# Optimization experiments

Hardware: AMD Instinct MI355X
Metric: run time of the kernel (lower is better)

Reference implementation:

```python
import jax, jax.numpy as jnp
import numpy as np

EPS = 1e-8  # matches torch F.cosine_similarity eps


def setup_inputs() -> dict:
    key = jax.random.key(0)
    S, U, D = 2048, 10, 256  # speakers, utterances/speaker, embedding dim
    embeddings = jax.random.normal(key, (S * U, D), dtype=jnp.float32)
    labels = jnp.repeat(jnp.arange(S, dtype=jnp.int64), U)  # speaker-blocked, as the view() assumes
    return {"embeddings": embeddings, "labels": labels}


def reference(embeddings, labels):
    labels_np = np.asarray(labels)
    S = int(np.unique(labels_np).size)          # num_speakers (static)
    B, D = embeddings.shape
    U = B // S                                   # num_utterances
    E = embeddings.reshape(S, U, D)
    C = E.mean(axis=1)                           # (S, D) centroids
    En = E / jnp.maximum(jnp.linalg.norm(E, axis=-1, keepdims=True), EPS)
    Cn = C / jnp.maximum(jnp.linalg.norm(C, axis=-1, keepdims=True), EPS)
    sim = jnp.einsum('sud,kd->suk', En, Cn)      # (S, U, S) cosine similarities
    idx = jnp.arange(S)
    pos = sim[idx, :, idx]                       # (S, U) similarity to own centroid
    neg_mask = jnp.eye(S, dtype=bool)[:, None, :]  # mask out k == i
    neg = jnp.where(neg_mask, -jnp.inf, sim)
    lse = jax.nn.logsumexp(neg, axis=-1)         # (S, U)
    loss = jnp.mean(-pos + lse)
    return loss
```

## Files before the change

### kernel.cpp

```cpp
#include <hip/hip_runtime.h>
#include <math.h>

#define SS   2048
#define UU   10
#define DD   256
#define BB   (SS * UU)
#define EPSF 1e-8f

typedef __attribute__((ext_vector_type(8))) short   bf16x8;
typedef __attribute__((ext_vector_type(4))) float   floatx4;

__device__ static inline unsigned short f2bf(float f) {
    union { float f; unsigned u; } v; v.f = f;
    unsigned r = (v.u + 0x7FFFu + ((v.u >> 16) & 1u)) >> 16;
    return (unsigned short)r;
}

__device__ static inline void gl_lds16(const unsigned short* g, unsigned short* l) {
    __builtin_amdgcn_global_load_lds((const __attribute__((address_space(1))) void*)g,
                                     (__attribute__((address_space(3))) void*)l, 16, 0, 0);
}

__global__ __launch_bounds__(256) void prep_kernel(const float* __restrict__ E,
                                                   unsigned short* __restrict__ Enb,
                                                   unsigned short* __restrict__ Cnb,
                                                   float* __restrict__ sumexp,
                                                   float* __restrict__ out) {
    const int s   = blockIdx.x;
    const int wid = threadIdx.x >> 6, lane = threadIdx.x & 63;
    __shared__ float cent[4][256];
    __shared__ float sred[256];

    if (threadIdx.x < UU) sumexp[s * UU + threadIdx.x] = 0.f;
    if (s == 0 && threadIdx.x == 0) out[0] = 0.f;

    float cp0 = 0.f, cp1 = 0.f, cp2 = 0.f, cp3 = 0.f;
    for (int u = wid; u < UU; u += 4) {
        const size_t roff = (size_t)(s * UU + u) * DD;
        float4 v = ((const float4*)(E + roff))[lane];
        float ssq = v.x * v.x + v.y * v.y + v.z * v.z + v.w * v.w;
#pragma unroll
        for (int off = 32; off; off >>= 1) ssq += __shfl_xor(ssq, off, 64);
        const float rinv = 1.0f / fmaxf(sqrtf(ssq), EPSF);
        ushort4 o;
        o.x = f2bf(v.x * rinv); o.y = f2bf(v.y * rinv);
        o.z = f2bf(v.z * rinv); o.w = f2bf(v.w * rinv);
        ((ushort4*)(Enb + roff))[lane] = o;
        cp0 += v.x; cp1 += v.y; cp2 += v.z; cp3 += v.w;
    }
    cent[wid][lane * 4 + 0] = cp0;
    cent[wid][lane * 4 + 1] = cp1;
    cent[wid][lane * 4 + 2] = cp2;
    cent[wid][lane * 4 + 3] = cp3;
    __syncthreads();

    const int d = threadIdx.x;
    const float c = (cent[0][d] + cent[1][d] + cent[2][d] + cent[3][d]) * 0.1f;
    sred[d] = c * c;
    __syncthreads();
#pragma unroll
    for (int off = 128; off; off >>= 1) {
        if (d < off) sred[d] += sred[d + off];
        __syncthreads();
    }
    const float rinv = 1.0f / fmaxf(sqrtf(sred[0]), EPSF);
    Cnb[(size_t)s * DD + d] = f2bf(c * rinv);
}

#define BM 128
#define BN 128
#define BK 32

__global__ __launch_bounds__(256) void gemm_lse_kernel(const unsigned short* __restrict__ Enb,
                                                       const unsigned short* __restrict__ Cnb,
                                                       float* __restrict__ posArr,
                                                       float* __restrict__ sumexp) {
    __shared__ unsigned short As[BM * BK];
    __shared__ unsigned short Bs[BN * BK];

    const int tid  = threadIdx.x;
    const int wid  = tid >> 6, lane = tid & 63;
    const int l15  = lane & 15, quad = lane >> 4;
    const int wave_m = wid >> 1, wave_n = wid & 1;

    const int bn = blockIdx.x & 15;
    const int bm = blockIdx.x >> 4;
    const int row0 = bm * BM, n0 = bn * BN;

    const int rl = lane >> 2;
    const int gf = ((lane & 3) ^ ((rl >> 1) & 3)) * 8;
    const unsigned short* gp[4];
    unsigned short* lp[4];
#pragma unroll
    for (int i = 0; i < 4; ++i) {
        const int c = wid * 4 + i;
        if (c < 8) {
            gp[i] = Enb + (size_t)(row0 + c * 16 + rl) * DD + gf;
            lp[i] = As + c * 512;
        } else {
            gp[i] = Cnb + (size_t)(n0 + (c - 8) * 16 + rl) * DD + gf;
            lp[i] = Bs + (c - 8) * 512;
        }
    }

    const int fswz = (quad ^ ((l15 >> 1) & 3)) * 8;
    int aoff[4], boff[4];
#pragma unroll
    for (int t = 0; t < 4; ++t) {
        aoff[t] = (wave_m * 64 + t * 16 + l15) * BK + fswz;
        boff[t] = (wave_n * 64 + t * 16 + l15) * BK + fswz;
    }

    floatx4 acc[4][4];
#pragma unroll
    for (int i = 0; i < 4; ++i)
#pragma unroll
        for (int j = 0; j < 4; ++j) acc[i][j] = (floatx4){0.f, 0.f, 0.f, 0.f};

    for (int k0 = 0; k0 < DD; k0 += BK) {
        __syncthreads();
#pragma unroll
        for (int i = 0; i < 4; ++i) gl_lds16(gp[i] + k0, lp[i]);
        __syncthreads();

        bf16x8 af[4], bfr[4];
#pragma unroll
        for (int t = 0; t < 4; ++t) af[t]  = *(const bf16x8*)(As + aoff[t]);
#pragma unroll
        for (int t = 0; t < 4; ++t) bfr[t] = *(const bf16x8*)(Bs + boff[t]);
#pragma unroll
        for (int mt = 0; mt < 4; ++mt)
#pragma unroll
            for (int nt = 0; nt < 4; ++nt)
                acc[mt][nt] = __builtin_amdgcn_mfma_f32_16x16x32_bf16(af[mt], bfr[nt], acc[mt][nt], 0, 0, 0);
    }

#pragma unroll
    for (int mt = 0; mt < 4; ++mt) {
        float rs[4] = {0.f, 0.f, 0.f, 0.f};
        const int growb = row0 + wave_m * 64 + mt * 16 + quad * 4;
#pragma unroll
        for (int nt = 0; nt < 4; ++nt) {
            const int col = n0 + wave_n * 64 + nt * 16 + l15;
#pragma unroll
            for (int r = 0; r < 4; ++r) {
                const int grow = growb + r;
                const float sim = acc[mt][nt][r];
                if (col == grow / UU) {
                    posArr[grow] = sim;
                } else {
                    rs[r] += __expf(sim);
                }
            }
        }
#pragma unroll
        for (int m = 1; m < 16; m <<= 1) {
#pragma unroll
            for (int r = 0; r < 4; ++r) rs[r] += __shfl_xor(rs[r], m, 64);
        }
        if (l15 == 0) {
#pragma unroll
            for (int r = 0; r < 4; ++r) atomicAdd(&sumexp[growb + r], rs[r]);
        }
    }
}

__global__ __launch_bounds__(256) void finalize_kernel(const float* __restrict__ posArr,
                                                       const float* __restrict__ sumexp,
                                                       float* __restrict__ out) {
    __shared__ float sred[256];
    const int tid = threadIdx.x;
    const int r = blockIdx.x * 256 + tid;
    sred[tid] = logf(sumexp[r]) - posArr[r];
    __syncthreads();
#pragma unroll
    for (int off = 128; off; off >>= 1) {
        if (tid < off) sred[tid] += sred[tid + off];
        __syncthreads();
    }
    if (tid == 0) atomicAdd(out, sred[0] * (1.0f / (float)BB));
}

extern "C" void kernel_launch(void* const* d_in, const int* in_sizes, int n_in,
                              void* d_out, int out_size, void* d_ws, size_t ws_size,
                              hipStream_t stream) {
    const float* E = (const float*)d_in[0];
    float* out = (float*)d_out;

    unsigned short* Enb = (unsigned short*)d_ws;
    unsigned short* Cnb = Enb + (size_t)BB * DD;
    float* posArr = (float*)(Cnb + (size_t)SS * DD);
    float* sumexp = posArr + BB;

    prep_kernel<<<SS, 256, 0, stream>>>(E, Enb, Cnb, sumexp, out);
    gemm_lse_kernel<<<(BB / BM) * (SS / BN), 256, 0, stream>>>(Enb, Cnb, posArr, sumexp);
    finalize_kernel<<<BB / 256, 256, 0, stream>>>(posArr, sumexp, out);
}
```

Before: 115.6 us.

## Preload full K into LDS and pipeline MFMA with per-chunk vmcnt waits

Each block now issues all eight K-chunk global→LDS loads up front into a 128 KB LDS buffer, then consumes chunks in order, waiting on vmcnt counters so MFMA work on early chunks overlaps the remaining loads. This removes the per-iteration load/sync serialization of the single-buffered loop. It also remaps block indices with a swizzle so that concurrently running blocks share A/B tiles, aiming for better L2 reuse. The large LDS footprint limits occupancy to about one block per CU.

```diff
diff --git a/kernel.cpp b/kernel.cpp
--- a/kernel.cpp
+++ b/kernel.cpp
@@ -70,21 +70,39 @@
 #define BM 128
 #define BN 128
 #define BK 32
+#define NCK 8
+
+__device__ __forceinline__ void chunk_mfma(const unsigned short* Ab,
+                                           const unsigned short* Bb,
+                                           const int* aoff, const int* boff,
+                                           floatx4 (&acc)[4][4]) {
+    bf16x8 af[4], bfr[4];
+#pragma unroll
+    for (int t = 0; t < 4; ++t) af[t]  = *(const bf16x8*)(Ab + aoff[t]);
+#pragma unroll
+    for (int t = 0; t < 4; ++t) bfr[t] = *(const bf16x8*)(Bb + boff[t]);
+#pragma unroll
+    for (int mt = 0; mt < 4; ++mt)
+#pragma unroll
+        for (int nt = 0; nt < 4; ++nt)
+            acc[mt][nt] = __builtin_amdgcn_mfma_f32_16x16x32_bf16(af[mt], bfr[nt], acc[mt][nt], 0, 0, 0);
+}
 
 __global__ __launch_bounds__(256) void gemm_lse_kernel(const unsigned short* __restrict__ Enb,
                                                        const unsigned short* __restrict__ Cnb,
                                                        float* __restrict__ posArr,
                                                        float* __restrict__ sumexp) {
-    __shared__ unsigned short As[BM * BK];
-    __shared__ unsigned short Bs[BN * BK];
+    __shared__ unsigned short As[NCK * BM * BK];
+    __shared__ unsigned short Bs[NCK * BN * BK];
 
     const int tid  = threadIdx.x;
     const int wid  = tid >> 6, lane = tid & 63;
     const int l15  = lane & 15, quad = lane >> 4;
     const int wave_m = wid >> 1, wave_n = wid & 1;
 
-    const int bn = blockIdx.x & 15;
-    const int bm = blockIdx.x >> 4;
+    const int swz = (blockIdx.x & 7) * 320 + (blockIdx.x >> 3);
+    const int bn = swz & 15;
+    const int bm = swz >> 4;
     const int row0 = bm * BM, n0 = bn * BN;
 
     const int rl = lane >> 2;
@@ -103,6 +121,13 @@
         }
     }
 
+#pragma unroll
+    for (int ck = 0; ck < NCK; ++ck) {
+#pragma unroll
+        for (int i = 0; i < 4; ++i)
+            gl_lds16(gp[i] + ck * BK, lp[i] + ck * (BM * BK));
+    }
+
     const int fswz = (quad ^ ((l15 >> 1) & 3)) * 8;
     int aoff[4], boff[4];
 #pragma unroll
@@ -117,23 +142,15 @@
 #pragma unroll
         for (int j = 0; j < 4; ++j) acc[i][j] = (floatx4){0.f, 0.f, 0.f, 0.f};
 
-    for (int k0 = 0; k0 < DD; k0 += BK) {
-        __syncthreads();
-#pragma unroll
-        for (int i = 0; i < 4; ++i) gl_lds16(gp[i] + k0, lp[i]);
-        __syncthreads();
-
-        bf16x8 af[4], bfr[4];
-#pragma unroll
-        for (int t = 0; t < 4; ++t) af[t]  = *(const bf16x8*)(As + aoff[t]);
-#pragma unroll
-        for (int t = 0; t < 4; ++t) bfr[t] = *(const bf16x8*)(Bs + boff[t]);
-#pragma unroll
-        for (int mt = 0; mt < 4; ++mt)
-#pragma unroll
-            for (int nt = 0; nt < 4; ++nt)
-                acc[mt][nt] = __builtin_amdgcn_mfma_f32_16x16x32_bf16(af[mt], bfr[nt], acc[mt][nt], 0, 0, 0);
-    }
+#define STEP(CK, VM)                                                        \
+    asm volatile("s_waitcnt vmcnt(" #VM ")" ::: "memory");                  \
+    __builtin_amdgcn_s_barrier();                                           \
+    __builtin_amdgcn_sched_barrier(0);                                      \
+    chunk_mfma(As + (CK) * (BM * BK), Bs + (CK) * (BN * BK), aoff, boff, acc);
+
+    STEP(0, 28) STEP(1, 24) STEP(2, 20) STEP(3, 16)
+    STEP(4, 12) STEP(5, 8)  STEP(6, 4)  STEP(7, 0)
+#undef STEP
 
 #pragma unroll
     for (int mt = 0; mt < 4; ++mt) {
```

Result: slower. 153.7 us (+33.0%).

## Rewrite GEMM-LSE with 256x256 tiles, double-buffered LDS pipeline, block swizzle

Applied to the files above, without the earlier changes.

The GEMM+logsumexp kernel moves from 128x128x32 tiles with 256 threads to 256x256x64 tiles with 512 threads. LDS is double-buffered, and each k-tile's global-to-LDS prefetch is issued in phases interleaved with MFMA work, using explicit barriers, waitcnts and setprio. The block index is remapped for locality and the per-row label division is hoisted out of the inner loop. The prep kernel's centroid norm reduction now uses wave shuffles instead of an LDS tree. The larger accumulator array raises register pressure and the hand-placed barriers must be exactly right, but the kernel should spend less time stalled on loads and syncs and reuse each tile more.

```diff
diff --git a/kernel.cpp b/kernel.cpp
--- a/kernel.cpp
+++ b/kernel.cpp
@@ -29,7 +29,7 @@
     const int s   = blockIdx.x;
     const int wid = threadIdx.x >> 6, lane = threadIdx.x & 63;
     __shared__ float cent[4][256];
-    __shared__ float sred[256];
+    __shared__ float part[4];
 
     if (threadIdx.x < UU) sumexp[s * UU + threadIdx.x] = 0.f;
     if (s == 0 && threadIdx.x == 0) out[0] = 0.f;
@@ -56,98 +56,129 @@
 
     const int d = threadIdx.x;
     const float c = (cent[0][d] + cent[1][d] + cent[2][d] + cent[3][d]) * 0.1f;
-    sred[d] = c * c;
+    float p = c * c;
+#pragma unroll
+    for (int off = 32; off; off >>= 1) p += __shfl_xor(p, off, 64);
+    if (lane == 0) part[wid] = p;
     __syncthreads();
-#pragma unroll
-    for (int off = 128; off; off >>= 1) {
-        if (d < off) sred[d] += sred[d + off];
-        __syncthreads();
-    }
-    const float rinv = 1.0f / fmaxf(sqrtf(sred[0]), EPSF);
+    const float tot = part[0] + part[1] + part[2] + part[3];
+    const float rinv = 1.0f / fmaxf(sqrtf(tot), EPSF);
     Cnb[(size_t)s * DD + d] = f2bf(c * rinv);
 }
 
-#define BM 128
-#define BN 128
-#define BK 32
-
-__global__ __launch_bounds__(256) void gemm_lse_kernel(const unsigned short* __restrict__ Enb,
-                                                       const unsigned short* __restrict__ Cnb,
-                                                       float* __restrict__ posArr,
-                                                       float* __restrict__ sumexp) {
-    __shared__ unsigned short As[BM * BK];
-    __shared__ unsigned short Bs[BN * BK];
+#define BMg 256
+#define BNg 256
+#define BKg 64
+#define NTg 4
+#define TSH (BMg * BKg)
+
+__global__ __launch_bounds__(512, 2) void gemm_lse_kernel(const unsigned short* __restrict__ Enb,
+                                                          const unsigned short* __restrict__ Cnb,
+                                                          float* __restrict__ posArr,
+                                                          float* __restrict__ sumexp) {
+    __shared__ unsigned short As[2 * TSH];
+    __shared__ unsigned short Bs[2 * TSH];
 
     const int tid  = threadIdx.x;
     const int wid  = tid >> 6, lane = tid & 63;
     const int l15  = lane & 15, quad = lane >> 4;
-    const int wave_m = wid >> 1, wave_n = wid & 1;
-
-    const int bn = blockIdx.x & 15;
-    const int bm = blockIdx.x >> 4;
-    const int row0 = bm * BM, n0 = bn * BN;
-
-    const int rl = lane >> 2;
-    const int gf = ((lane & 3) ^ ((rl >> 1) & 3)) * 8;
-    const unsigned short* gp[4];
-    unsigned short* lp[4];
+    const int wave_m = wid >> 2, wave_n = wid & 3;
+
+    const int swz = (blockIdx.x & 7) * 80 + (blockIdx.x >> 3);
+    const int bn = swz & 7;
+    const int bm = swz >> 3;
+    const int row0 = bm * BMg, n0 = bn * BNg;
+
+    const int rl8 = lane >> 3, gl = lane & 7;
+    const unsigned short *gpa[4], *gpb[4];
+    int lof[4];
 #pragma unroll
     for (int i = 0; i < 4; ++i) {
-        const int c = wid * 4 + i;
-        if (c < 8) {
-            gp[i] = Enb + (size_t)(row0 + c * 16 + rl) * DD + gf;
-            lp[i] = As + c * 512;
-        } else {
-            gp[i] = Cnb + (size_t)(n0 + (c - 8) * 16 + rl) * DD + gf;
-            lp[i] = Bs + (c - 8) * 512;
-        }
-    }
-
-    const int fswz = (quad ^ ((l15 >> 1) & 3)) * 8;
-    int aoff[4], boff[4];
-#pragma unroll
-    for (int t = 0; t < 4; ++t) {
-        aoff[t] = (wave_m * 64 + t * 16 + l15) * BK + fswz;
-        boff[t] = (wave_n * 64 + t * 16 + l15) * BK + fswz;
-    }
-
-    floatx4 acc[4][4];
-#pragma unroll
-    for (int i = 0; i < 4; ++i)
+        const int rw  = wid * 32 + i * 8 + rl8;
+        const int gsw = (gl ^ (rw & 7)) * 8;
+        gpa[i] = Enb + (size_t)(row0 + rw) * DD + gsw;
+        gpb[i] = Cnb + (size_t)(n0  + rw) * DD + gsw;
+        lof[i] = (wid * 32 + i * 8) * 64;
+    }
+
+#define STAGE_A(T) { _Pragma("unroll") for (int i_ = 0; i_ < 4; ++i_) \
+        gl_lds16(gpa[i_] + (T) * BKg, As + ((T) & 1) * TSH + lof[i_]); }
+#define STAGE_B(T) { _Pragma("unroll") for (int i_ = 0; i_ < 4; ++i_) \
+        gl_lds16(gpb[i_] + (T) * BKg, Bs + ((T) & 1) * TSH + lof[i_]); }
+
+    const int swq  = l15 & 7;
+    const int arow = wave_m * 128 + l15;
+    const int brow = wave_n * 64 + l15;
+
+    floatx4 acc[8][4];
+#pragma unroll
+    for (int i = 0; i < 8; ++i)
 #pragma unroll
         for (int j = 0; j < 4; ++j) acc[i][j] = (floatx4){0.f, 0.f, 0.f, 0.f};
 
-    for (int k0 = 0; k0 < DD; k0 += BK) {
-        __syncthreads();
-#pragma unroll
-        for (int i = 0; i < 4; ++i) gl_lds16(gp[i] + k0, lp[i]);
-        __syncthreads();
-
-        bf16x8 af[4], bfr[4];
-#pragma unroll
-        for (int t = 0; t < 4; ++t) af[t]  = *(const bf16x8*)(As + aoff[t]);
-#pragma unroll
-        for (int t = 0; t < 4; ++t) bfr[t] = *(const bf16x8*)(Bs + boff[t]);
-#pragma unroll
-        for (int mt = 0; mt < 4; ++mt)
-#pragma unroll
-            for (int nt = 0; nt < 4; ++nt)
-                acc[mt][nt] = __builtin_amdgcn_mfma_f32_16x16x32_bf16(af[mt], bfr[nt], acc[mt][nt], 0, 0, 0);
-    }
-
-#pragma unroll
-    for (int mt = 0; mt < 4; ++mt) {
+#define PHASE(T, P, SA, SB, BOUND)                                            \
+  {                                                                           \
+    bf16x8 af_[4], bf_[4];                                                    \
+    _Pragma("unroll")                                                         \
+    for (int mt = 0; mt < 4; ++mt)                                            \
+      af_[mt] = *(const bf16x8*)(As + ((T) & 1) * TSH +                       \
+                 (arow + ((P) & 1) * 64 + mt * 16) * 64 +                     \
+                 ((((P) >> 1) * 4 + quad) ^ swq) * 8);                        \
+    _Pragma("unroll")                                                         \
+    for (int nt = 0; nt < 4; ++nt)                                            \
+      bf_[nt] = *(const bf16x8*)(Bs + ((T) & 1) * TSH +                       \
+                 (brow + nt * 16) * 64 +                                      \
+                 ((((P) >> 1) * 4 + quad) ^ swq) * 8);                        \
+    if (SA) STAGE_A((T) + 1);                                                 \
+    if (SB) STAGE_B((T) + 1);                                                 \
+    __builtin_amdgcn_s_barrier();                                             \
+    asm volatile("s_waitcnt lgkmcnt(0)" ::: "memory");                        \
+    __builtin_amdgcn_sched_barrier(0);                                        \
+    __builtin_amdgcn_s_setprio(1);                                            \
+    _Pragma("unroll")                                                         \
+    for (int mt = 0; mt < 4; ++mt)                                            \
+      _Pragma("unroll")                                                       \
+      for (int nt = 0; nt < 4; ++nt)                                          \
+        acc[((P) & 1) * 4 + mt][nt] = __builtin_amdgcn_mfma_f32_16x16x32_bf16(\
+            af_[mt], bf_[nt], acc[((P) & 1) * 4 + mt][nt], 0, 0, 0);          \
+    __builtin_amdgcn_s_setprio(0);                                            \
+    if (BOUND) {                                                              \
+      asm volatile("s_waitcnt vmcnt(0)" ::: "memory");                        \
+      __builtin_amdgcn_s_barrier();                                           \
+      __builtin_amdgcn_sched_barrier(0);                                      \
+    } else {                                                                  \
+      __builtin_amdgcn_s_barrier();                                           \
+    }                                                                         \
+  }
+
+    STAGE_A(0); STAGE_B(0);
+    asm volatile("s_waitcnt vmcnt(0)" ::: "memory");
+    __builtin_amdgcn_s_barrier();
+    __builtin_amdgcn_sched_barrier(0);
+
+    PHASE(0, 0, 1, 0, 0) PHASE(0, 1, 0, 1, 0) PHASE(0, 2, 0, 0, 0) PHASE(0, 3, 0, 0, 1)
+    PHASE(1, 0, 1, 0, 0) PHASE(1, 1, 0, 1, 0) PHASE(1, 2, 0, 0, 0) PHASE(1, 3, 0, 0, 1)
+    PHASE(2, 0, 1, 0, 0) PHASE(2, 1, 0, 1, 0) PHASE(2, 2, 0, 0, 0) PHASE(2, 3, 0, 0, 1)
+    PHASE(3, 0, 0, 0, 0) PHASE(3, 1, 0, 0, 0) PHASE(3, 2, 0, 0, 0) PHASE(3, 3, 0, 0, 0)
+#undef PHASE
+#undef STAGE_A
+#undef STAGE_B
+
+#pragma unroll
+    for (int mt = 0; mt < 8; ++mt) {
+        const int growb = row0 + wave_m * 128 + mt * 16 + quad * 4;
         float rs[4] = {0.f, 0.f, 0.f, 0.f};
-        const int growb = row0 + wave_m * 64 + mt * 16 + quad * 4;
+        int lbl[4];
+#pragma unroll
+        for (int r = 0; r < 4; ++r) lbl[r] = (growb + r) / UU;
 #pragma unroll
         for (int nt = 0; nt < 4; ++nt) {
             const int col = n0 + wave_n * 64 + nt * 16 + l15;
 #pragma unroll
             for (int r = 0; r < 4; ++r) {
-                const int grow = growb + r;
                 const float sim = acc[mt][nt][r];
-                if (col == grow / UU) {
-                    posArr[grow] = sim;
+                if (col == lbl[r]) {
+                    posArr[growb + r] = sim;
                 } else {
                     rs[r] += __expf(sim);
                 }
@@ -193,6 +224,6 @@
     float* sumexp = posArr + BB;
 
     prep_kernel<<<SS, 256, 0, stream>>>(E, Enb, Cnb, sumexp, out);
-    gemm_lse_kernel<<<(BB / BM) * (SS / BN), 256, 0, stream>>>(Enb, Cnb, posArr, sumexp);
+    gemm_lse_kernel<<<(BB / BMg) * (SS / BNg), 512, 0, stream>>>(Enb, Cnb, posArr, sumexp);
     finalize_kernel<<<BB / 256, 256, 0, stream>>>(posArr, sumexp, out);
 }
```

After: 121.9 us. +5.5%, slower.

## Restructure GEMM-LSE to keep full-K row tile in LDS and stream centroids from global

Applied to the files above, without the earlier changes.

Each block now loads a 128x256 bf16 row tile of normalized embeddings into LDS once, using an XOR swizzle. Each wave sweeps 128 centroid columns with operands read directly from global memory and register double-buffered. This replaces the per-K-step LDS staging and two barriers per step. Per-row exp sums are reduced into LDS, so each block issues one global atomic per row instead of many, and a block-index swizzle is added for locality. The prep kernel's centroid norm reduction switches from an LDS tree to wave shuffles. The cost is a large LDS footprint (64KB) that limits occupancy, and uncached global B loads that may stall the MFMAs.

```diff
diff --git a/kernel.cpp b/kernel.cpp
--- a/kernel.cpp
+++ b/kernel.cpp
@@ -14,11 +14,6 @@
     union { float f; unsigned u; } v; v.f = f;
     unsigned r = (v.u + 0x7FFFu + ((v.u >> 16) & 1u)) >> 16;
     return (unsigned short)r;
-}
-
-__device__ static inline void gl_lds16(const unsigned short* g, unsigned short* l) {
-    __builtin_amdgcn_global_load_lds((const __attribute__((address_space(1))) void*)g,
-                                     (__attribute__((address_space(3))) void*)l, 16, 0, 0);
 }
 
 __global__ __launch_bounds__(256) void prep_kernel(const float* __restrict__ E,
@@ -29,7 +24,7 @@
     const int s   = blockIdx.x;
     const int wid = threadIdx.x >> 6, lane = threadIdx.x & 63;
     __shared__ float cent[4][256];
-    __shared__ float sred[256];
+    __shared__ float part[4];
 
     if (threadIdx.x < UU) sumexp[s * UU + threadIdx.x] = 0.f;
     if (s == 0 && threadIdx.x == 0) out[0] = 0.f;
@@ -56,113 +51,127 @@
 
     const int d = threadIdx.x;
     const float c = (cent[0][d] + cent[1][d] + cent[2][d] + cent[3][d]) * 0.1f;
-    sred[d] = c * c;
-    __syncthreads();
-#pragma unroll
-    for (int off = 128; off; off >>= 1) {
-        if (d < off) sred[d] += sred[d + off];
-        __syncthreads();
-    }
-    const float rinv = 1.0f / fmaxf(sqrtf(sred[0]), EPSF);
+    float p = c * c;
+#pragma unroll
+    for (int off = 32; off; off >>= 1) p += __shfl_xor(p, off, 64);
+    if (lane == 0) part[wid] = p;
+    __syncthreads();
+    const float tot = part[0] + part[1] + part[2] + part[3];
+    const float rinv = 1.0f / fmaxf(sqrtf(tot), EPSF);
     Cnb[(size_t)s * DD + d] = f2bf(c * rinv);
 }
 
-#define BM 128
-#define BN 128
-#define BK 32
+#define RWS  128
+#define CBLK 512
+#define CT   64
 
 __global__ __launch_bounds__(256) void gemm_lse_kernel(const unsigned short* __restrict__ Enb,
                                                        const unsigned short* __restrict__ Cnb,
                                                        float* __restrict__ posArr,
                                                        float* __restrict__ sumexp) {
-    __shared__ unsigned short As[BM * BK];
-    __shared__ unsigned short Bs[BN * BK];
+    __shared__ unsigned short As[RWS * DD];
+    __shared__ float lsum[RWS];
 
     const int tid  = threadIdx.x;
     const int wid  = tid >> 6, lane = tid & 63;
     const int l15  = lane & 15, quad = lane >> 4;
-    const int wave_m = wid >> 1, wave_n = wid & 1;
-
-    const int bn = blockIdx.x & 15;
-    const int bm = blockIdx.x >> 4;
-    const int row0 = bm * BM, n0 = bn * BN;
-
-    const int rl = lane >> 2;
-    const int gf = ((lane & 3) ^ ((rl >> 1) & 3)) * 8;
-    const unsigned short* gp[4];
-    unsigned short* lp[4];
-#pragma unroll
-    for (int i = 0; i < 4; ++i) {
-        const int c = wid * 4 + i;
-        if (c < 8) {
-            gp[i] = Enb + (size_t)(row0 + c * 16 + rl) * DD + gf;
-            lp[i] = As + c * 512;
-        } else {
-            gp[i] = Cnb + (size_t)(n0 + (c - 8) * 16 + rl) * DD + gf;
-            lp[i] = Bs + (c - 8) * 512;
+
+    const int swz = (blockIdx.x & 7) * 80 + (blockIdx.x >> 3);
+    const int gb = swz >> 2;
+    const int cb = swz & 3;
+    const int row0 = gb * RWS;
+    const int n0   = cb * CBLK;
+
+    if (tid < RWS) lsum[tid] = 0.f;
+
+    {
+        const int ar = tid >> 1, ah = tid & 1;
+        const unsigned short* gsrc = Enb + (size_t)(row0 + ar) * DD + ah * 128;
+        unsigned short* lbase = As + ar * 256;
+#pragma unroll
+        for (int j = 0; j < 16; ++j) {
+            const int slot = (ah * 16 + j) ^ (ar & 15);
+            *(int4*)(lbase + slot * 8) = *(const int4*)(gsrc + j * 8);
         }
     }
-
-    const int fswz = (quad ^ ((l15 >> 1) & 3)) * 8;
-    int aoff[4], boff[4];
-#pragma unroll
-    for (int t = 0; t < 4; ++t) {
-        aoff[t] = (wave_m * 64 + t * 16 + l15) * BK + fswz;
-        boff[t] = (wave_n * 64 + t * 16 + l15) * BK + fswz;
-    }
-
-    floatx4 acc[4][4];
-#pragma unroll
-    for (int i = 0; i < 4; ++i)
-#pragma unroll
-        for (int j = 0; j < 4; ++j) acc[i][j] = (floatx4){0.f, 0.f, 0.f, 0.f};
-
-    for (int k0 = 0; k0 < DD; k0 += BK) {
-        __syncthreads();
-#pragma unroll
-        for (int i = 0; i < 4; ++i) gl_lds16(gp[i] + k0, lp[i]);
-        __syncthreads();
-
-        bf16x8 af[4], bfr[4];
-#pragma unroll
-        for (int t = 0; t < 4; ++t) af[t]  = *(const bf16x8*)(As + aoff[t]);
-#pragma unroll
-        for (int t = 0; t < 4; ++t) bfr[t] = *(const bf16x8*)(Bs + boff[t]);
-#pragma unroll
-        for (int mt = 0; mt < 4; ++mt)
-#pragma unroll
-            for (int nt = 0; nt < 4; ++nt)
-                acc[mt][nt] = __builtin_amdgcn_mfma_f32_16x16x32_bf16(af[mt], bfr[nt], acc[mt][nt], 0, 0, 0);
-    }
-
-#pragma unroll
-    for (int mt = 0; mt < 4; ++mt) {
-        float rs[4] = {0.f, 0.f, 0.f, 0.f};
-        const int growb = row0 + wave_m * 64 + mt * 16 + quad * 4;
-#pragma unroll
-        for (int nt = 0; nt < 4; ++nt) {
-            const int col = n0 + wave_n * 64 + nt * 16 + l15;
-#pragma unroll
-            for (int r = 0; r < 4; ++r) {
-                const int grow = growb + r;
-                const float sim = acc[mt][nt][r];
-                if (col == grow / UU) {
-                    posArr[grow] = sim;
-                } else {
-                    rs[r] += __expf(sim);
+    __syncthreads();
+
+    const int wc0 = n0 + wid * (2 * CT);
+
+#pragma unroll
+    for (int c = 0; c < 2; ++c) {
+        const int ct0 = wc0 + c * CT;
+
+        floatx4 acc[8][4];
+#pragma unroll
+        for (int i = 0; i < 8; ++i)
+#pragma unroll
+            for (int j = 0; j < 4; ++j) acc[i][j] = (floatx4){0.f, 0.f, 0.f, 0.f};
+
+        const unsigned short* bbase[4];
+#pragma unroll
+        for (int nt = 0; nt < 4; ++nt)
+            bbase[nt] = Cnb + (size_t)(ct0 + nt * 16 + l15) * DD + quad * 8;
+
+        bf16x8 bb[2][4];
+#pragma unroll
+        for (int nt = 0; nt < 4; ++nt) bb[0][nt] = *(const bf16x8*)(bbase[nt]);
+
+#pragma unroll
+        for (int kk = 0; kk < 8; ++kk) {
+            if (kk < 7) {
+#pragma unroll
+                for (int nt = 0; nt < 4; ++nt)
+                    bb[(kk + 1) & 1][nt] = *(const bf16x8*)(bbase[nt] + (kk + 1) * 32);
+            }
+            bf16x8 af[8];
+#pragma unroll
+            for (int mt = 0; mt < 8; ++mt)
+                af[mt] = *(const bf16x8*)(As + (mt * 16 + l15) * 256 +
+                                          (((kk * 4 + quad) ^ l15) * 8));
+#pragma unroll
+            for (int mt = 0; mt < 8; ++mt)
+#pragma unroll
+                for (int nt = 0; nt < 4; ++nt)
+                    acc[mt][nt] = __builtin_amdgcn_mfma_f32_16x16x32_bf16(
+                        af[mt], bb[kk & 1][nt], acc[mt][nt], 0, 0, 0);
+        }
+
+#pragma unroll
+        for (int mt = 0; mt < 8; ++mt) {
+            const int growb = row0 + mt * 16 + quad * 4;
+            float rs[4] = {0.f, 0.f, 0.f, 0.f};
+            int lbl[4];
+#pragma unroll
+            for (int r = 0; r < 4; ++r) lbl[r] = (growb + r) / UU;
+#pragma unroll
+            for (int nt = 0; nt < 4; ++nt) {
+                const int col = ct0 + nt * 16 + l15;
+#pragma unroll
+                for (int r = 0; r < 4; ++r) {
+                    const float sim = acc[mt][nt][r];
+                    if (col == lbl[r]) {
+                        posArr[growb + r] = sim;
+                    } else {
+                        rs[r] += __expf(sim);
+                    }
                 }
             }
+#pragma unroll
+            for (int m = 1; m < 16; m <<= 1) {
+#pragma unroll
+                for (int r = 0; r < 4; ++r) rs[r] += __shfl_xor(rs[r], m, 64);
+            }
+            if (l15 == 0) {
+#pragma unroll
+                for (int r = 0; r < 4; ++r)
+                    atomicAdd(&lsum[mt * 16 + quad * 4 + r], rs[r]);
+            }
         }
-#pragma unroll
-        for (int m = 1; m < 16; m <<= 1) {
-#pragma unroll
-            for (int r = 0; r < 4; ++r) rs[r] += __shfl_xor(rs[r], m, 64);
-        }
-        if (l15 == 0) {
-#pragma unroll
-            for (int r = 0; r < 4; ++r) atomicAdd(&sumexp[growb + r], rs[r]);
-        }
-    }
+    }
+
+    __syncthreads();
+    if (tid < RWS) atomicAdd(&sumexp[row0 + tid], lsum[tid]);
 }
 
 __global__ __launch_bounds__(256) void finalize_kernel(const float* __restrict__ posArr,
@@ -193,6 +202,6 @@
     float* sumexp = posArr + BB;
 
     prep_kernel<<<SS, 256, 0, stream>>>(E, Enb, Cnb, sumexp, out);
-    gemm_lse_kernel<<<(BB / BM) * (SS / BN), 256, 0, stream>>>(Enb, Cnb, posArr, sumexp);
+    gemm_lse_kernel<<<(BB / RWS) * (SS / CBLK), 256, 0, stream>>>(Enb, Cnb, posArr, sumexp);
     finalize_kernel<<<BB / 256, 256, 0, stream>>>(posArr, sumexp, out);
 }
```

New measurement: 147.5 us. +27.6%, slower.
